# Optimization experiments

Hardware: AMD Instinct MI355X
Metric: run time of the kernel (lower is better)

Reference implementation:

```python
import math
import jax, jax.numpy as jnp
import numpy as np

B, N, D, H, NUM_N, NUM_J = 16, 1024, 128, 8, 8, 4
PRE_S = 2.0


def setup_inputs() -> dict:
    key = jax.random.key(0)
    ks = jax.random.split(key, 12)
    g = lambda i, shape: jax.random.normal(ks[i], shape, jnp.float32) * 0.02
    return {
        "eigenvector": jax.random.normal(ks[0], (B, N, N), jnp.float32),
        "eigenvalue": jax.random.uniform(ks[1], (B, N), jnp.float32, minval=0.0, maxval=2.0),
        "length": jax.random.randint(ks[2], (B,), N // 2, N).at[0].set(N),
        "eig_w_W": g(3, (D, D + 1)), "eig_w_b": jnp.zeros((D,), jnp.float32),
        "ln1_s": jnp.ones((D,), jnp.float32), "ln1_b": jnp.zeros((D,), jnp.float32),
        "ln2_s": jnp.ones((D,), jnp.float32), "ln2_b": jnp.zeros((D,), jnp.float32),
        "qkv_W": g(4, (3 * D, D)), "qkv_b": jnp.zeros((3 * D,), jnp.float32),
        "out_W": g(5, (D, D)), "out_b": jnp.zeros((D,), jnp.float32),
        "ffn_W1": g(6, (D, D)), "ffn_b1": jnp.zeros((D,), jnp.float32),
        "ffn_W2": g(7, (D, D)), "ffn_b2": jnp.zeros((D,), jnp.float32),
        "dec_sca_W": g(8, (NUM_N, D)), "dec_sca_b": jnp.zeros((NUM_N,), jnp.float32),
        "dec_wav_W": g(9, (NUM_N, D)), "dec_wav_b": jnp.zeros((NUM_N,), jnp.float32),
        "dec_scl_W": g(10, (NUM_J, D)), "dec_scl_b": jnp.zeros((NUM_J,), jnp.float32),
    }


def _layernorm(x, s, b):
    m = x.mean(-1, keepdims=True)
    v = ((x - m) ** 2).mean(-1, keepdims=True)
    return (x - m) / jnp.sqrt(v + 1e-5) * s + b


def _gen_base(y, num_n):
    # Chebyshev-style recurrence; returns (base_wavelet, base_scaling), each [B, num_n, ...y.shape[1:]]
    t_even = jnp.ones_like(y)
    t_odd = y
    wav, sca = [t_even], [t_odd]
    for _ in range(num_n - 1):
        t_even = 2.0 * y * t_odd - t_even
        t_odd = 2.0 * y * t_even - t_odd
        wav.append(t_even)
        sca.append(t_odd)
    return jnp.stack(wav, 1), jnp.stack(sca, 1)


def _forward(eigenvalue, length,
             eig_w_W, eig_w_b, ln1_s, ln1_b, ln2_s, ln2_b,
             qkv_W, qkv_b, out_W, out_b, ffn_W1, ffn_b1, ffn_W2, ffn_b2,
             dec_sca_W, dec_sca_b, dec_wav_W, dec_wav_b, dec_scl_W, dec_scl_b):
    eva = eigenvalue  # [B, N], max(length) == N by construction
    pad = jnp.arange(N)[None, :] >= length[:, None]  # [B, N], True = padded key

    # --- SineEncoding ---
    div = jnp.exp(jnp.arange(0, D, 2).astype(jnp.float32) * (-math.log(10000.0) / D))  # [D/2]
    pe = (eva * 100.0)[:, :, None] * div  # [B, N, D/2]
    eeig = jnp.concatenate([eva[:, :, None], jnp.sin(pe), jnp.cos(pe)], -1)  # [B, N, D+1]
    eig = eeig @ eig_w_W.T + eig_w_b  # [B, N, D]

    # --- MHA block (pre-norm, key padding mask) ---
    h = _layernorm(eig, ln1_s, ln1_b)
    q, k, v = jnp.split(h @ qkv_W.T + qkv_b, 3, axis=-1)
    dh = D // H
    rh = lambda t: t.reshape(B, N, H, dh)
    scores = jnp.einsum('bqhd,bkhd->bhqk', rh(q), rh(k)) / math.sqrt(dh)
    scores = jnp.where(pad[:, None, None, :], -1e9, scores)  # finite mask (padded rows zeroed later)
    attn = jax.nn.softmax(scores, axis=-1)
    mo = jnp.einsum('bhqk,bkhd->bqhd', attn, rh(v)).reshape(B, N, D) @ out_W.T + out_b
    eig = eig + mo

    # --- FFN block ---
    f = _layernorm(eig, ln2_s, ln2_b)
    f = jax.nn.gelu(f @ ffn_W1.T + ffn_b1, approximate=False) @ ffn_W2.T + ffn_b2
    eig = eig + f

    lenf = length.astype(jnp.float32)[:, None]

    def pooled(W, b):
        c = eig @ W.T + b
        c = jnp.where(pad[:, :, None], 0.0, c)
        return c.sum(1) / (lenf + 1e-8)

    coe_sca = jax.nn.sigmoid(pooled(dec_sca_W, dec_sca_b))  # [B, NUM_N]
    coe_sca = coe_sca / (coe_sca.sum(-1, keepdims=True) + 1e-8)
    coe_wav = jax.nn.sigmoid(pooled(dec_wav_W, dec_wav_b))
    coe_wav = coe_wav / (coe_wav.sum(-1, keepdims=True) + 1e-8)
    coe_scl = jax.nn.sigmoid(pooled(dec_scl_W, dec_scl_b)) * PRE_S  # [B, NUM_J]

    _, base_scaling = _gen_base(eva[:, :, None] - 1.0, NUM_N)  # [B, NUM_N, N, 1]
    fsw = eva[:, :, None] * coe_scl[:, None, :]  # [B, N, NUM_J]
    fsw = jnp.where(fsw > 2.0, 0.0, fsw)
    base_wavelet, _ = _gen_base(fsw - 1.0, NUM_N)  # [B, NUM_N, N, NUM_J]

    base_scaling = 0.5 * (1.0 - base_scaling)
    base_wavelet = 0.5 * (1.0 - base_wavelet)
    curr_s = jnp.einsum('bn,bnxj->bxj', coe_sca, base_scaling)  # [B, N, 1]
    curr_w = jnp.einsum('bn,bnxj->bxj', coe_wav, base_wavelet)  # [B, N, NUM_J]
    out = jnp.concatenate([curr_s, curr_w], -1)  # [B, N, 1+NUM_J]
    out = out / (jnp.linalg.norm(out, axis=-1, keepdims=True) + 1e-8)  # tight_frames
    return out


def reference(eigenvector, eigenvalue, length,
              eig_w_W, eig_w_b, ln1_s, ln1_b, ln2_s, ln2_b,
              qkv_W, qkv_b, out_W, out_b, ffn_W1, ffn_b1, ffn_W2, ffn_b2,
              dec_sca_W, dec_sca_b, dec_wav_W, dec_wav_b, dec_scl_W, dec_scl_b):
    # eigenvector (evc_dense) is passed through unchanged in the original; the learned
    # output is filter_signals_after, which we return.
    return _forward(eigenvalue, length,
                    eig_w_W, eig_w_b, ln1_s, ln1_b, ln2_s, ln2_b,
                    qkv_W, qkv_b, out_W, out_b, ffn_W1, ffn_b1, ffn_W2, ffn_b2,
                    dec_sca_W, dec_sca_b, dec_wav_W, dec_wav_b, dec_scl_W, dec_scl_b)
```

## Files before the change

### kernel.cpp

```cpp
#include <hip/hip_runtime.h>
#include <math.h>

#define NB 16
#define NN 1024
#define ND 128
#define NH 8
#define DH 16

typedef float f32x4 __attribute__((ext_vector_type(4)));
typedef short s16x4 __attribute__((ext_vector_type(4)));

static __device__ __forceinline__ ushort f2bf(float x) {
  unsigned u = __float_as_uint(x);
  u = (u + 0x7FFFu + ((u >> 16) & 1u)) >> 16;
  return (ushort)u;
}

static __device__ __forceinline__ float exp2h(float x) {
  return __builtin_amdgcn_exp2f(x);
}

static __device__ __forceinline__ f32x4 mfma16(s16x4 a, s16x4 b, f32x4 c) {
  return __builtin_amdgcn_mfma_f32_16x16x16bf16_1k(a, b, c, 0, 0, 0);
}

static __device__ __forceinline__ s16x4 pack_bf4(float p0, float p1, float p2,
                                                 float p3) {
  s16x4 r = {(short)f2bf(p0), (short)f2bf(p1), (short)f2bf(p2),
             (short)f2bf(p3)};
  return r;
}

#define QSCALE 0.36067376022224085f

__global__ __launch_bounds__(256) void kW(
    const float* __restrict__ eW, const float* __restrict__ qkvW,
    const float* __restrict__ outW, const float* __restrict__ W1,
    const float* __restrict__ W2, ushort* __restrict__ wbf) {
  int i = blockIdx.x * 256 + threadIdx.x;
  if (i < 18432) {
    int r = i / 144, k = i - r * 144;
    wbf[i] = (k < 129) ? f2bf(eW[r * 129 + k]) : (ushort)0;
  } else if (i < 67584) {
    wbf[i] = f2bf(qkvW[i - 18432]);
  } else if (i < 83968) {
    wbf[i] = f2bf(outW[i - 67584]);
  } else if (i < 100352) {
    wbf[i] = f2bf(W1[i - 83968]);
  } else if (i < 116736) {
    wbf[i] = f2bf(W2[i - 100352]);
  }
}

__global__ __launch_bounds__(256, 4) void kA(
    const float* __restrict__ eva, const ushort* __restrict__ eWbf,
    const float* __restrict__ eb, const float* __restrict__ g1s,
    const float* __restrict__ g1b, const ushort* __restrict__ qkvbf,
    const float* __restrict__ qb, float* __restrict__ eig,
    ushort* __restrict__ qg, ushort* __restrict__ kg,
    ushort* __restrict__ vt) {
  __shared__ __align__(16) ushort ee[32][148];
  __shared__ __align__(16) float eig_f[32][132];
  __shared__ __align__(16) ushort hbf[32][132];
  int t = threadIdx.x;
  int rows0 = blockIdx.x * 32;
  int w = t >> 6, l = t & 63, g = l >> 4, c = l & 15;

  {
    int d = t & 63, r0 = t >> 6;
    float div = __expf((float)(2 * d) * (-9.210340371976184f / 128.0f));
#pragma unroll
    for (int k = 0; k < 8; ++k) {
      int row = r0 + 4 * k;
      float e = eva[rows0 + row];
      float pe = e * 100.0f * div;
      ee[row][1 + d] = f2bf(__sinf(pe));
      ee[row][65 + d] = f2bf(__cosf(pe));
      if (d == 0) ee[row][0] = f2bf(e);
    }
  }
  for (int i = t; i < 32 * 19; i += 256) {
    int row = i / 19, cc = 129 + (i - row * 19);
    ee[row][cc] = 0;
  }
  __syncthreads();

  {
    int rt = w >> 1;
#pragma unroll
    for (int i = 0; i < 4; ++i) {
      int ct = (w & 1) * 4 + i;
      f32x4 st = {0.f, 0.f, 0.f, 0.f};
#pragma unroll
      for (int kk = 0; kk < 9; ++kk) {
        s16x4 xf = *(const s16x4*)&ee[rt * 16 + c][kk * 16 + g * 4];
        s16x4 yf = *(const s16x4*)&eWbf[(ct * 16 + c) * 144 + kk * 16 + g * 4];
        st = mfma16(xf, yf, st);
      }
      float bias = eb[ct * 16 + c];
#pragma unroll
      for (int j = 0; j < 4; ++j)
        eig_f[rt * 16 + g * 4 + j][ct * 16 + c] = st[j] + bias;
    }
  }
  __syncthreads();

#pragma unroll
  for (int p = 0; p < 4; ++p) {
    int idx = p * 256 + t;
    int row = idx >> 5, c4 = idx & 31;
    *(float4*)&eig[(size_t)(rows0 + row) * ND + c4 * 4] =
        *(const float4*)&eig_f[row][c4 * 4];
  }

  {
    int row = t >> 3, s = t & 7;
    float vals[16];
    float sum = 0.f;
#pragma unroll
    for (int k = 0; k < 16; ++k) {
      vals[k] = eig_f[row][s + 8 * k];
      sum += vals[k];
    }
    sum += __shfl_xor(sum, 1, 8);
    sum += __shfl_xor(sum, 2, 8);
    sum += __shfl_xor(sum, 4, 8);
    float mean = sum * (1.0f / 128.0f);
    float sq = 0.f;
#pragma unroll
    for (int k = 0; k < 16; ++k) {
      float d = vals[k] - mean;
      sq += d * d;
    }
    sq += __shfl_xor(sq, 1, 8);
    sq += __shfl_xor(sq, 2, 8);
    sq += __shfl_xor(sq, 4, 8);
    float rstd = rsqrtf(sq * (1.0f / 128.0f) + 1e-5f);
#pragma unroll
    for (int k = 0; k < 16; ++k) {
      int col = s + 8 * k;
      hbf[row][col] = f2bf((vals[k] - mean) * rstd * g1s[col] + g1b[col]);
    }
  }
  __syncthreads();

  {
    int rt = w >> 1;
    int b = rows0 >> 10, nn0 = rows0 & 1023;
#pragma unroll
    for (int i = 0; i < 12; ++i) {
      int ct = (w & 1) * 12 + i;
      f32x4 st = {0.f, 0.f, 0.f, 0.f};
#pragma unroll
      for (int kk = 0; kk < 8; ++kk) {
        s16x4 xf = *(const s16x4*)&hbf[rt * 16 + c][kk * 16 + g * 4];
        s16x4 yf = *(const s16x4*)&qkvbf[(ct * 16 + c) * 128 + kk * 16 + g * 4];
        st = mfma16(xf, yf, st);
      }
      float bias = qb[ct * 16 + c];
      int which = ct >> 3, head = ct & 7;
      if (which == 2) {
        unsigned lo = (unsigned)f2bf(st[0] + bias) |
                      ((unsigned)f2bf(st[1] + bias) << 16);
        unsigned hi = (unsigned)f2bf(st[2] + bias) |
                      ((unsigned)f2bf(st[3] + bias) << 16);
        uint2 pk;
        pk.x = lo;
        pk.y = hi;
        *(uint2*)(vt + ((size_t)(b * NH + head) * DH + c) * NN + nn0 +
                  rt * 16 + g * 4) = pk;
      } else {
        ushort* dst = which == 0 ? qg : kg;
        float sc = which == 0 ? QSCALE : 1.0f;
        size_t base =
            ((size_t)(b * NH + head) * NN + nn0 + rt * 16 + g * 4) * DH + c;
#pragma unroll
        for (int j = 0; j < 4; ++j)
          dst[base + j * DH] = f2bf((st[j] + bias) * sc);
      }
    }
  }
}

__global__ __launch_bounds__(512) void k_attn(
    const ushort* __restrict__ qg, const ushort* __restrict__ kg,
    const ushort* __restrict__ vt, const int* __restrict__ length,
    ushort* __restrict__ att) {
  __shared__ ushort Ksh[2][128][20];
  __shared__ ushort VTsh[2][16][136];
  int bid = blockIdx.x;
  int bh = bid >> 3, qc = bid & 7;
  int b = bh >> 3, h = bh & 7;
  int t = threadIdx.x;
  int w = t >> 6, l = t & 63, g = l >> 4, c = l & 15;
  int len = length[b];
  int nt = (len + 127) >> 7;
  int qrow = qc * 128 + w * 16 + c;
  s16x4 qf = *(const s16x4*)(qg + ((size_t)bh * NN + qrow) * DH + g * 4);
  f32x4 oacc0 = {0.f, 0.f, 0.f, 0.f};
  f32x4 oacc1 = {0.f, 0.f, 0.f, 0.f};
  float lsum = 0.f;
  int ksr = t >> 2, ksc = t & 3;
  int vr = t >> 5, vc = t & 31;
  const ushort* kbg = kg + (size_t)bh * NN * DH;
  const ushort* vbg = vt + (size_t)bh * DH * NN;

  {
    uint2 kv = *(const uint2*)(kbg + (size_t)ksr * DH + ksc * 4);
    uint2 vv = *(const uint2*)(vbg + (size_t)vr * NN + vc * 4);
    *(uint2*)&Ksh[0][ksr][ksc * 4] = kv;
    *(uint2*)&VTsh[0][vr][vc * 4] = vv;
  }
  __syncthreads();

  int cur = 0;
  for (int ti = 0; ti < nt; ++ti) {
    int t0 = ti << 7;
    bool pre = (ti + 1 < nt);
    uint2 kvn = {0u, 0u}, vvn = {0u, 0u};
    if (pre) {
      int t1 = t0 + 128;
      kvn = *(const uint2*)(kbg + (size_t)(t1 + ksr) * DH + ksc * 4);
      vvn = *(const uint2*)(vbg + (size_t)vr * NN + t1 + vc * 4);
    }
    if (t0 + 128 <= len) {
      __builtin_amdgcn_s_setprio(1);
#pragma unroll
      for (int kt = 0; kt < 8; ++kt) {
        s16x4 kf = *(const s16x4*)&Ksh[cur][kt * 16 + c][g * 4];
        f32x4 st = {0.f, 0.f, 0.f, 0.f};
        st = mfma16(kf, qf, st);
        float p0 = exp2h(st[0]), p1 = exp2h(st[1]);
        float p2 = exp2h(st[2]), p3 = exp2h(st[3]);
        lsum += (p0 + p1) + (p2 + p3);
        s16x4 pf = pack_bf4(p0, p1, p2, p3);
        s16x4 vf = *(const s16x4*)&VTsh[cur][c][kt * 16 + g * 4];
        if (kt & 1) oacc1 = mfma16(vf, pf, oacc1);
        else oacc0 = mfma16(vf, pf, oacc0);
      }
      __builtin_amdgcn_s_setprio(0);
    } else {
      for (int kt = 0; kt < 8 && t0 + kt * 16 < len; ++kt) {
        s16x4 kf = *(const s16x4*)&Ksh[cur][kt * 16 + c][g * 4];
        f32x4 st = {0.f, 0.f, 0.f, 0.f};
        st = mfma16(kf, qf, st);
        int kj = t0 + kt * 16 + g * 4;
        float p0 = (kj + 0 < len) ? exp2h(st[0]) : 0.f;
        float p1 = (kj + 1 < len) ? exp2h(st[1]) : 0.f;
        float p2 = (kj + 2 < len) ? exp2h(st[2]) : 0.f;
        float p3 = (kj + 3 < len) ? exp2h(st[3]) : 0.f;
        lsum += (p0 + p1) + (p2 + p3);
        s16x4 pf = pack_bf4(p0, p1, p2, p3);
        s16x4 vf = *(const s16x4*)&VTsh[cur][c][kt * 16 + g * 4];
        if (kt & 1) oacc1 = mfma16(vf, pf, oacc1);
        else oacc0 = mfma16(vf, pf, oacc0);
      }
    }
    if (pre) {
      *(uint2*)&Ksh[cur ^ 1][ksr][ksc * 4] = kvn;
      *(uint2*)&VTsh[cur ^ 1][vr][vc * 4] = vvn;
      __syncthreads();
      cur ^= 1;
    }
  }
  f32x4 oacc = {oacc0[0] + oacc1[0], oacc0[1] + oacc1[1],
                oacc0[2] + oacc1[2], oacc0[3] + oacc1[3]};
  lsum += __shfl_xor(lsum, 16, 64);
  lsum += __shfl_xor(lsum, 32, 64);
  float inv = 1.0f / lsum;
  s16x4 ob = pack_bf4(oacc[0] * inv, oacc[1] * inv, oacc[2] * inv,
                      oacc[3] * inv);
  *(s16x4*)(att + ((size_t)b * NN + qrow) * ND + h * DH + g * 4) = ob;
}

__global__ __launch_bounds__(256, 4) void kB(
    const ushort* __restrict__ attg, const ushort* __restrict__ outbf,
    const float* __restrict__ ob, const float* __restrict__ g2s,
    const float* __restrict__ g2b, const ushort* __restrict__ w1bf,
    const float* __restrict__ fb1, const ushort* __restrict__ w2bf,
    const float* __restrict__ fb2, const float* __restrict__ eig,
    const int* __restrict__ length, float* __restrict__ bsum) {
  __shared__ __align__(16) ushort attb[32][136];
  __shared__ __align__(16) float eig_f[32][132];
  __shared__ __align__(16) ushort hbf[32][132];
  __shared__ float csum[2][128];
  int t = threadIdx.x;
  int rows0 = blockIdx.x * 32;
  int w = t >> 6, l = t & 63, g = l >> 4, c = l & 15;
  int rt = w >> 1;

#pragma unroll
  for (int p = 0; p < 2; ++p) {
    int idx = p * 256 + t;
    int row = idx >> 4, c8 = idx & 15;
    *(uint4*)&attb[row][c8 * 8] =
        *(const uint4*)&attg[(size_t)(rows0 + row) * ND + c8 * 8];
  }
#pragma unroll
  for (int p = 0; p < 4; ++p) {
    int idx = p * 256 + t;
    int row = idx >> 5, c4 = idx & 31;
    *(float4*)&eig_f[row][c4 * 4] =
        *(const float4*)&eig[(size_t)(rows0 + row) * ND + c4 * 4];
  }
  __syncthreads();

#pragma unroll
  for (int i = 0; i < 4; ++i) {
    int ct = (w & 1) * 4 + i;
    f32x4 st = {0.f, 0.f, 0.f, 0.f};
#pragma unroll
    for (int kk = 0; kk < 8; ++kk) {
      s16x4 xf = *(const s16x4*)&attb[rt * 16 + c][kk * 16 + g * 4];
      s16x4 yf = *(const s16x4*)&outbf[(ct * 16 + c) * 128 + kk * 16 + g * 4];
      st = mfma16(xf, yf, st);
    }
    float bias = ob[ct * 16 + c];
#pragma unroll
    for (int j = 0; j < 4; ++j) {
      int row = rt * 16 + g * 4 + j, col = ct * 16 + c;
      eig_f[row][col] = st[j] + bias + eig_f[row][col];
    }
  }
  __syncthreads();

  {
    int row = t >> 3, s = t & 7;
    float vals[16];
    float sum = 0.f;
#pragma unroll
    for (int k = 0; k < 16; ++k) {
      vals[k] = eig_f[row][s + 8 * k];
      sum += vals[k];
    }
    sum += __shfl_xor(sum, 1, 8);
    sum += __shfl_xor(sum, 2, 8);
    sum += __shfl_xor(sum, 4, 8);
    float mean = sum * (1.0f / 128.0f);
    float sq = 0.f;
#pragma unroll
    for (int k = 0; k < 16; ++k) {
      float d = vals[k] - mean;
      sq += d * d;
    }
    sq += __shfl_xor(sq, 1, 8);
    sq += __shfl_xor(sq, 2, 8);
    sq += __shfl_xor(sq, 4, 8);
    float rstd = rsqrtf(sq * (1.0f / 128.0f) + 1e-5f);
#pragma unroll
    for (int k = 0; k < 16; ++k) {
      int col = s + 8 * k;
      hbf[row][col] = f2bf((vals[k] - mean) * rstd * g2s[col] + g2b[col]);
    }
  }
  __syncthreads();

#pragma unroll
  for (int i = 0; i < 4; ++i) {
    int ct = (w & 1) * 4 + i;
    f32x4 st = {0.f, 0.f, 0.f, 0.f};
#pragma unroll
    for (int kk = 0; kk < 8; ++kk) {
      s16x4 xf = *(const s16x4*)&hbf[rt * 16 + c][kk * 16 + g * 4];
      s16x4 yf = *(const s16x4*)&w1bf[(ct * 16 + c) * 128 + kk * 16 + g * 4];
      st = mfma16(xf, yf, st);
    }
    float bias = fb1[ct * 16 + c];
#pragma unroll
    for (int j = 0; j < 4; ++j) {
      float gv = st[j] + bias;
      attb[rt * 16 + g * 4 + j][ct * 16 + c] =
          f2bf(0.5f * gv * (1.0f + erff(gv * 0.7071067811865475f)));
    }
  }
  __syncthreads();

#pragma unroll
  for (int i = 0; i < 4; ++i) {
    int ct = (w & 1) * 4 + i;
    f32x4 st = {0.f, 0.f, 0.f, 0.f};
#pragma unroll
    for (int kk = 0; kk < 8; ++kk) {
      s16x4 xf = *(const s16x4*)&attb[rt * 16 + c][kk * 16 + g * 4];
      s16x4 yf = *(const s16x4*)&w2bf[(ct * 16 + c) * 128 + kk * 16 + g * 4];
      st = mfma16(xf, yf, st);
    }
    float bias = fb2[ct * 16 + c];
#pragma unroll
    for (int j = 0; j < 4; ++j) {
      int row = rt * 16 + g * 4 + j, col = ct * 16 + c;
      eig_f[row][col] = st[j] + bias + eig_f[row][col];
    }
  }
  __syncthreads();

  {
    int b = rows0 >> 10, n0 = rows0 & 1023;
    int len = length[b];
    int col = t & 127, half = t >> 7;
    float s = 0.f;
#pragma unroll
    for (int r = 0; r < 16; ++r) {
      int row = half * 16 + r;
      if (n0 + row < len) s += eig_f[row][col];
    }
    csum[half][col] = s;
  }
  __syncthreads();
  if (t < 128) bsum[(size_t)blockIdx.x * 128 + t] = csum[0][t] + csum[1][t];
}

__global__ __launch_bounds__(128) void kE(
    const float* __restrict__ bsum, const int* __restrict__ length,
    const float* __restrict__ dsW, const float* __restrict__ dsB,
    const float* __restrict__ dwW, const float* __restrict__ dwB,
    const float* __restrict__ dlW, const float* __restrict__ dlB,
    float* __restrict__ coe) {
  int b = blockIdx.x, t = threadIdx.x;
  __shared__ float s[128];
  __shared__ float pg[20];
  __shared__ float nrm[2];
  float a = 0.f;
#pragma unroll
  for (int c = 0; c < 32; ++c) a += bsum[(size_t)(b * 32 + c) * 128 + t];
  s[t] = a;
  __syncthreads();
  if (t < 20) {
    const float* W = t < 8 ? dsW + t * 128
                           : (t < 16 ? dwW + (t - 8) * 128 : dlW + (t - 16) * 128);
    float bias = t < 8 ? dsB[t] : (t < 16 ? dwB[t - 8] : dlB[t - 16]);
    float d = 0.f;
    for (int j = 0; j < 128; ++j) d += s[j] * W[j];
    float lf = (float)length[b];
    float pooled = (d + lf * bias) / (lf + 1e-8f);
    pg[t] = 1.f / (1.f + expf(-pooled));
  }
  __syncthreads();
  if (t == 0) {
    float a1 = 0.f, a2 = 0.f;
    for (int i = 0; i < 8; ++i) a1 += pg[i];
    for (int i = 8; i < 16; ++i) a2 += pg[i];
    nrm[0] = a1 + 1e-8f;
    nrm[1] = a2 + 1e-8f;
  }
  __syncthreads();
  if (t < 8) coe[b * 20 + t] = pg[t] / nrm[0];
  else if (t < 16) coe[b * 20 + t] = pg[t] / nrm[1];
  else if (t < 20) coe[b * 20 + t] = pg[t] * 2.0f;
}

__global__ __launch_bounds__(256) void k_wave(const float* __restrict__ eva,
                                              const float* __restrict__ coe,
                                              float* __restrict__ out) {
  int bn = blockIdx.x * 256 + threadIdx.x;
  int b = bn >> 10;
  float e = eva[bn];
  const float* cb = coe + b * 20;
  float y = e - 1.0f;
  float te = 1.0f, to = y;
  float cs = cb[0] * 0.5f * (1.0f - to);
#pragma unroll
  for (int i = 1; i < 8; ++i) {
    te = 2.f * y * to - te;
    to = 2.f * y * te - to;
    cs += cb[i] * 0.5f * (1.0f - to);
  }
  float cw[4];
#pragma unroll
  for (int j = 0; j < 4; ++j) {
    float fs = e * cb[16 + j];
    fs = (fs > 2.0f) ? 0.0f : fs;
    float yw = fs - 1.0f;
    float te2 = 1.0f, to2 = yw;
    float acc = 0.0f;
#pragma unroll
    for (int i = 1; i < 8; ++i) {
      te2 = 2.f * yw * to2 - te2;
      to2 = 2.f * yw * te2 - to2;
      acc += cb[8 + i] * 0.5f * (1.0f - te2);
    }
    cw[j] = acc;
  }
  float nrm = cs * cs + cw[0] * cw[0] + cw[1] * cw[1] + cw[2] * cw[2] +
              cw[3] * cw[3];
  float inv = 1.0f / (sqrtf(nrm) + 1e-8f);
  float* o = out + bn * 5;
  o[0] = cs * inv;
  o[1] = cw[0] * inv;
  o[2] = cw[1] * inv;
  o[3] = cw[2] * inv;
  o[4] = cw[3] * inv;
}

extern "C" void kernel_launch(void* const* d_in, const int* in_sizes, int n_in,
                              void* d_out, int out_size, void* d_ws,
                              size_t ws_size, hipStream_t stream) {
  const float* eva = (const float*)d_in[1];
  const int* length = (const int*)d_in[2];
  const float* eig_w_W = (const float*)d_in[3];
  const float* eig_w_b = (const float*)d_in[4];
  const float* ln1_s = (const float*)d_in[5];
  const float* ln1_b = (const float*)d_in[6];
  const float* ln2_s = (const float*)d_in[7];
  const float* ln2_b = (const float*)d_in[8];
  const float* qkv_W = (const float*)d_in[9];
  const float* qkv_b = (const float*)d_in[10];
  const float* out_W = (const float*)d_in[11];
  const float* out_b = (const float*)d_in[12];
  const float* ffn_W1 = (const float*)d_in[13];
  const float* ffn_b1 = (const float*)d_in[14];
  const float* ffn_W2 = (const float*)d_in[15];
  const float* ffn_b2 = (const float*)d_in[16];
  const float* dec_sca_W = (const float*)d_in[17];
  const float* dec_sca_b = (const float*)d_in[18];
  const float* dec_wav_W = (const float*)d_in[19];
  const float* dec_wav_b = (const float*)d_in[20];
  const float* dec_scl_W = (const float*)d_in[21];
  const float* dec_scl_b = (const float*)d_in[22];

  float* ws = (float*)d_ws;
  const size_t SZ = (size_t)NB * NN * ND;
  float* eig = ws;
  ushort* qg = (ushort*)(ws + SZ);
  ushort* kg = qg + SZ;
  ushort* vt = kg + SZ;
  ushort* attg = vt + SZ;
  float* bsum = (float*)(attg + SZ);
  float* coe = bsum + 512 * 128;
  ushort* wbf = (ushort*)(coe + 512);
  ushort* eWbf = wbf;
  ushort* qkvbf = wbf + 18432;
  ushort* outbf = wbf + 67584;
  ushort* w1bf = wbf + 83968;
  ushort* w2bf = wbf + 100352;

  kW<<<(116736 + 255) / 256, 256, 0, stream>>>(eig_w_W, qkv_W, out_W, ffn_W1,
                                               ffn_W2, wbf);
  kA<<<NB * NN / 32, 256, 0, stream>>>(eva, eWbf, eig_w_b, ln1_s, ln1_b, qkvbf,
                                       qkv_b, eig, qg, kg, vt);
  k_attn<<<NB * NH * 8, 512, 0, stream>>>(qg, kg, vt, length, attg);
  kB<<<NB * NN / 32, 256, 0, stream>>>(attg, outbf, out_b, ln2_s, ln2_b, w1bf,
                                       ffn_b1, w2bf, ffn_b2, eig, length, bsum);
  kE<<<NB, 128, 0, stream>>>(bsum, length, dec_sca_W, dec_sca_b, dec_wav_W,
                             dec_wav_b, dec_scl_W, dec_scl_b, coe);
  k_wave<<<(NB * NN) / 256, 256, 0, stream>>>(eva, coe, (float*)d_out);
}
```

Baseline: 100.2 us.

## Halve row tiles in kA/kB, use tanh GELU, fuse decoder into wave kernel

kA and kB now process 16 rows per block instead of 32, which doubles the grid and raises the occupancy hint, so more blocks are in flight. Each block reloads the bf16 weights for half as many rows, which adds weight traffic. The exact erf GELU is replaced by a tanh approximation built on exp2, which changes numerics. The kE coefficient kernel is merged into k_wave, saving one launch but making each of the four blocks per batch recompute the bsum reduction and decoder.

```diff
diff --git a/kernel.cpp b/kernel.cpp
--- a/kernel.cpp
+++ b/kernel.cpp
@@ -18,6 +18,15 @@
 
 static __device__ __forceinline__ float exp2h(float x) {
   return __builtin_amdgcn_exp2f(x);
+}
+
+static __device__ __forceinline__ float gelu_f(float x) {
+  float u = 0.7978845608028654f * (x + 0.044715f * x * x * x);
+  float au = fabsf(u);
+  float tex = exp2h(-2.8853900817779268f * au);
+  float th = (1.0f - tex) / (1.0f + tex);
+  th = copysignf(th, u);
+  return 0.5f * x * (1.0f + th);
 }
 
 static __device__ __forceinline__ f32x4 mfma16(s16x4 a, s16x4 b, f32x4 c) {
@@ -52,25 +61,25 @@
   }
 }
 
-__global__ __launch_bounds__(256, 4) void kA(
+__global__ __launch_bounds__(256, 6) void kA(
     const float* __restrict__ eva, const ushort* __restrict__ eWbf,
     const float* __restrict__ eb, const float* __restrict__ g1s,
     const float* __restrict__ g1b, const ushort* __restrict__ qkvbf,
     const float* __restrict__ qb, float* __restrict__ eig,
     ushort* __restrict__ qg, ushort* __restrict__ kg,
     ushort* __restrict__ vt) {
-  __shared__ __align__(16) ushort ee[32][148];
-  __shared__ __align__(16) float eig_f[32][132];
-  __shared__ __align__(16) ushort hbf[32][132];
+  __shared__ __align__(16) ushort ee[16][148];
+  __shared__ __align__(16) float eig_f[16][132];
+  __shared__ __align__(16) ushort hbf[16][132];
   int t = threadIdx.x;
-  int rows0 = blockIdx.x * 32;
+  int rows0 = blockIdx.x * 16;
   int w = t >> 6, l = t & 63, g = l >> 4, c = l & 15;
 
   {
     int d = t & 63, r0 = t >> 6;
     float div = __expf((float)(2 * d) * (-9.210340371976184f / 128.0f));
 #pragma unroll
-    for (int k = 0; k < 8; ++k) {
+    for (int k = 0; k < 4; ++k) {
       int row = r0 + 4 * k;
       float e = eva[rows0 + row];
       float pe = e * 100.0f * div;
@@ -79,34 +88,31 @@
       if (d == 0) ee[row][0] = f2bf(e);
     }
   }
-  for (int i = t; i < 32 * 19; i += 256) {
+  for (int i = t; i < 16 * 19; i += 256) {
     int row = i / 19, cc = 129 + (i - row * 19);
     ee[row][cc] = 0;
   }
   __syncthreads();
 
-  {
-    int rt = w >> 1;
-#pragma unroll
-    for (int i = 0; i < 4; ++i) {
-      int ct = (w & 1) * 4 + i;
-      f32x4 st = {0.f, 0.f, 0.f, 0.f};
-#pragma unroll
-      for (int kk = 0; kk < 9; ++kk) {
-        s16x4 xf = *(const s16x4*)&ee[rt * 16 + c][kk * 16 + g * 4];
-        s16x4 yf = *(const s16x4*)&eWbf[(ct * 16 + c) * 144 + kk * 16 + g * 4];
-        st = mfma16(xf, yf, st);
-      }
-      float bias = eb[ct * 16 + c];
-#pragma unroll
-      for (int j = 0; j < 4; ++j)
-        eig_f[rt * 16 + g * 4 + j][ct * 16 + c] = st[j] + bias;
-    }
-  }
-  __syncthreads();
-
-#pragma unroll
-  for (int p = 0; p < 4; ++p) {
+#pragma unroll
+  for (int i = 0; i < 2; ++i) {
+    int ct = w * 2 + i;
+    f32x4 st = {0.f, 0.f, 0.f, 0.f};
+#pragma unroll
+    for (int kk = 0; kk < 9; ++kk) {
+      s16x4 xf = *(const s16x4*)&ee[c][kk * 16 + g * 4];
+      s16x4 yf = *(const s16x4*)&eWbf[(ct * 16 + c) * 144 + kk * 16 + g * 4];
+      st = mfma16(xf, yf, st);
+    }
+    float bias = eb[ct * 16 + c];
+#pragma unroll
+    for (int j = 0; j < 4; ++j)
+      eig_f[g * 4 + j][ct * 16 + c] = st[j] + bias;
+  }
+  __syncthreads();
+
+#pragma unroll
+  for (int p = 0; p < 2; ++p) {
     int idx = p * 256 + t;
     int row = idx >> 5, c4 = idx & 31;
     *(float4*)&eig[(size_t)(rows0 + row) * ND + c4 * 4] =
@@ -114,46 +120,47 @@
   }
 
   {
-    int row = t >> 3, s = t & 7;
-    float vals[16];
+    int row = t >> 4, s = t & 15;
+    float vals[8];
     float sum = 0.f;
 #pragma unroll
-    for (int k = 0; k < 16; ++k) {
-      vals[k] = eig_f[row][s + 8 * k];
+    for (int k = 0; k < 8; ++k) {
+      vals[k] = eig_f[row][s + 16 * k];
       sum += vals[k];
     }
-    sum += __shfl_xor(sum, 1, 8);
-    sum += __shfl_xor(sum, 2, 8);
-    sum += __shfl_xor(sum, 4, 8);
+    sum += __shfl_xor(sum, 1, 16);
+    sum += __shfl_xor(sum, 2, 16);
+    sum += __shfl_xor(sum, 4, 16);
+    sum += __shfl_xor(sum, 8, 16);
     float mean = sum * (1.0f / 128.0f);
     float sq = 0.f;
 #pragma unroll
-    for (int k = 0; k < 16; ++k) {
+    for (int k = 0; k < 8; ++k) {
       float d = vals[k] - mean;
       sq += d * d;
     }
-    sq += __shfl_xor(sq, 1, 8);
-    sq += __shfl_xor(sq, 2, 8);
-    sq += __shfl_xor(sq, 4, 8);
+    sq += __shfl_xor(sq, 1, 16);
+    sq += __shfl_xor(sq, 2, 16);
+    sq += __shfl_xor(sq, 4, 16);
+    sq += __shfl_xor(sq, 8, 16);
     float rstd = rsqrtf(sq * (1.0f / 128.0f) + 1e-5f);
 #pragma unroll
-    for (int k = 0; k < 16; ++k) {
-      int col = s + 8 * k;
+    for (int k = 0; k < 8; ++k) {
+      int col = s + 16 * k;
       hbf[row][col] = f2bf((vals[k] - mean) * rstd * g1s[col] + g1b[col]);
     }
   }
   __syncthreads();
 
   {
-    int rt = w >> 1;
     int b = rows0 >> 10, nn0 = rows0 & 1023;
 #pragma unroll
-    for (int i = 0; i < 12; ++i) {
-      int ct = (w & 1) * 12 + i;
+    for (int i = 0; i < 6; ++i) {
+      int ct = w * 6 + i;
       f32x4 st = {0.f, 0.f, 0.f, 0.f};
 #pragma unroll
       for (int kk = 0; kk < 8; ++kk) {
-        s16x4 xf = *(const s16x4*)&hbf[rt * 16 + c][kk * 16 + g * 4];
+        s16x4 xf = *(const s16x4*)&hbf[c][kk * 16 + g * 4];
         s16x4 yf = *(const s16x4*)&qkvbf[(ct * 16 + c) * 128 + kk * 16 + g * 4];
         st = mfma16(xf, yf, st);
       }
@@ -167,13 +174,12 @@
         uint2 pk;
         pk.x = lo;
         pk.y = hi;
-        *(uint2*)(vt + ((size_t)(b * NH + head) * DH + c) * NN + nn0 +
-                  rt * 16 + g * 4) = pk;
+        *(uint2*)(vt + ((size_t)(b * NH + head) * DH + c) * NN + nn0 + g * 4) =
+            pk;
       } else {
         ushort* dst = which == 0 ? qg : kg;
         float sc = which == 0 ? QSCALE : 1.0f;
-        size_t base =
-            ((size_t)(b * NH + head) * NN + nn0 + rt * 16 + g * 4) * DH + c;
+        size_t base = ((size_t)(b * NH + head) * NN + nn0 + g * 4) * DH + c;
 #pragma unroll
         for (int j = 0; j < 4; ++j)
           dst[base + j * DH] = f2bf((st[j] + bias) * sc);
@@ -273,31 +279,28 @@
   *(s16x4*)(att + ((size_t)b * NN + qrow) * ND + h * DH + g * 4) = ob;
 }
 
-__global__ __launch_bounds__(256, 4) void kB(
+__global__ __launch_bounds__(256, 6) void kB(
     const ushort* __restrict__ attg, const ushort* __restrict__ outbf,
     const float* __restrict__ ob, const float* __restrict__ g2s,
     const float* __restrict__ g2b, const ushort* __restrict__ w1bf,
     const float* __restrict__ fb1, const ushort* __restrict__ w2bf,
     const float* __restrict__ fb2, const float* __restrict__ eig,
     const int* __restrict__ length, float* __restrict__ bsum) {
-  __shared__ __align__(16) ushort attb[32][136];
-  __shared__ __align__(16) float eig_f[32][132];
-  __shared__ __align__(16) ushort hbf[32][132];
+  __shared__ __align__(16) ushort attb[16][136];
+  __shared__ __align__(16) float eig_f[16][132];
+  __shared__ __align__(16) ushort hbf[16][132];
   __shared__ float csum[2][128];
   int t = threadIdx.x;
-  int rows0 = blockIdx.x * 32;
+  int rows0 = blockIdx.x * 16;
   int w = t >> 6, l = t & 63, g = l >> 4, c = l & 15;
-  int rt = w >> 1;
-
-#pragma unroll
-  for (int p = 0; p < 2; ++p) {
-    int idx = p * 256 + t;
-    int row = idx >> 4, c8 = idx & 15;
+
+  {
+    int row = t >> 4, c8 = t & 15;
     *(uint4*)&attb[row][c8 * 8] =
         *(const uint4*)&attg[(size_t)(rows0 + row) * ND + c8 * 8];
   }
 #pragma unroll
-  for (int p = 0; p < 4; ++p) {
+  for (int p = 0; p < 2; ++p) {
     int idx = p * 256 + t;
     int row = idx >> 5, c4 = idx & 31;
     *(float4*)&eig_f[row][c4 * 4] =
@@ -306,89 +309,88 @@
   __syncthreads();
 
 #pragma unroll
-  for (int i = 0; i < 4; ++i) {
-    int ct = (w & 1) * 4 + i;
+  for (int i = 0; i < 2; ++i) {
+    int ct = w * 2 + i;
     f32x4 st = {0.f, 0.f, 0.f, 0.f};
 #pragma unroll
     for (int kk = 0; kk < 8; ++kk) {
-      s16x4 xf = *(const s16x4*)&attb[rt * 16 + c][kk * 16 + g * 4];
+      s16x4 xf = *(const s16x4*)&attb[c][kk * 16 + g * 4];
       s16x4 yf = *(const s16x4*)&outbf[(ct * 16 + c) * 128 + kk * 16 + g * 4];
       st = mfma16(xf, yf, st);
     }
     float bias = ob[ct * 16 + c];
 #pragma unroll
     for (int j = 0; j < 4; ++j) {
-      int row = rt * 16 + g * 4 + j, col = ct * 16 + c;
+      int row = g * 4 + j, col = ct * 16 + c;
       eig_f[row][col] = st[j] + bias + eig_f[row][col];
     }
   }
   __syncthreads();
 
   {
-    int row = t >> 3, s = t & 7;
-    float vals[16];
+    int row = t >> 4, s = t & 15;
+    float vals[8];
     float sum = 0.f;
 #pragma unroll
-    for (int k = 0; k < 16; ++k) {
-      vals[k] = eig_f[row][s + 8 * k];
+    for (int k = 0; k < 8; ++k) {
+      vals[k] = eig_f[row][s + 16 * k];
       sum += vals[k];
     }
-    sum += __shfl_xor(sum, 1, 8);
-    sum += __shfl_xor(sum, 2, 8);
-    sum += __shfl_xor(sum, 4, 8);
+    sum += __shfl_xor(sum, 1, 16);
+    sum += __shfl_xor(sum, 2, 16);
+    sum += __shfl_xor(sum, 4, 16);
+    sum += __shfl_xor(sum, 8, 16);
     float mean = sum * (1.0f / 128.0f);
     float sq = 0.f;
 #pragma unroll
-    for (int k = 0; k < 16; ++k) {
+    for (int k = 0; k < 8; ++k) {
       float d = vals[k] - mean;
       sq += d * d;
     }
-    sq += __shfl_xor(sq, 1, 8);
-    sq += __shfl_xor(sq, 2, 8);
-    sq += __shfl_xor(sq, 4, 8);
+    sq += __shfl_xor(sq, 1, 16);
+    sq += __shfl_xor(sq, 2, 16);
+    sq += __shfl_xor(sq, 4, 16);
+    sq += __shfl_xor(sq, 8, 16);
     float rstd = rsqrtf(sq * (1.0f / 128.0f) + 1e-5f);
 #pragma unroll
-    for (int k = 0; k < 16; ++k) {
-      int col = s + 8 * k;
+    for (int k = 0; k < 8; ++k) {
+      int col = s + 16 * k;
       hbf[row][col] = f2bf((vals[k] - mean) * rstd * g2s[col] + g2b[col]);
     }
   }
   __syncthreads();
 
 #pragma unroll
-  for (int i = 0; i < 4; ++i) {
-    int ct = (w & 1) * 4 + i;
+  for (int i = 0; i < 2; ++i) {
+    int ct = w * 2 + i;
     f32x4 st = {0.f, 0.f, 0.f, 0.f};
 #pragma unroll
     for (int kk = 0; kk < 8; ++kk) {
-      s16x4 xf = *(const s16x4*)&hbf[rt * 16 + c][kk * 16 + g * 4];
+      s16x4 xf = *(const s16x4*)&hbf[c][kk * 16 + g * 4];
       s16x4 yf = *(const s16x4*)&w1bf[(ct * 16 + c) * 128 + kk * 16 + g * 4];
       st = mfma16(xf, yf, st);
     }
     float bias = fb1[ct * 16 + c];
 #pragma unroll
-    for (int j = 0; j < 4; ++j) {
-      float gv = st[j] + bias;
-      attb[rt * 16 + g * 4 + j][ct * 16 + c] =
-          f2bf(0.5f * gv * (1.0f + erff(gv * 0.7071067811865475f)));
-    }
-  }
-  __syncthreads();
-
-#pragma unroll
-  for (int i = 0; i < 4; ++i) {
-    int ct = (w & 1) * 4 + i;
+    for (int j = 0; j < 4; ++j)
+      attb[g * 4 + j][ct * 16 + c] = f2bf(gelu_f(st[j] + bias));
+  }
+  __syncthreads();
+
+#pragma unroll
+  for (int i = 0; i < 2; ++i) {
+    int ct = w * 2 + i;
     f32x4 st = {0.f, 0.f, 0.f, 0.f};
 #pragma unroll
     for (int kk = 0; kk < 8; ++kk) {
-      s16x4 xf = *(const s16x4*)&attb[rt * 16 + c][kk * 16 + g * 4];
+      s16x4 xf = *(const s16x4*)&attb[c][kk * 16 + g * 4];
       s16x4 yf = *(const s16x4*)&w2bf[(ct * 16 + c) * 128 + kk * 16 + g * 4];
       st = mfma16(xf, yf, st);
     }
     float bias = fb2[ct * 16 + c];
 #pragma unroll
     for (int j = 0; j < 4; ++j) {
-      int row = rt * 16 + g * 4 + j, col = ct * 16 + c;
+      int row = g * 4 + j, col = ct * 16 + c;
       eig_f[row][col] = st[j] + bias + eig_f[row][col];
     }
   }
@@ -400,8 +402,8 @@
     int col = t & 127, half = t >> 7;
     float s = 0.f;
 #pragma unroll
-    for (int r = 0; r < 16; ++r) {
-      int row = half * 16 + r;
+    for (int r = 0; r < 8; ++r) {
+      int row = half * 8 + r;
       if (n0 + row < len) s += eig_f[row][col];
     }
     csum[half][col] = s;
@@ -410,20 +412,24 @@
   if (t < 128) bsum[(size_t)blockIdx.x * 128 + t] = csum[0][t] + csum[1][t];
 }
 
-__global__ __launch_bounds__(128) void kE(
-    const float* __restrict__ bsum, const int* __restrict__ length,
-    const float* __restrict__ dsW, const float* __restrict__ dsB,
-    const float* __restrict__ dwW, const float* __restrict__ dwB,
-    const float* __restrict__ dlW, const float* __restrict__ dlB,
-    float* __restrict__ coe) {
-  int b = blockIdx.x, t = threadIdx.x;
+__global__ __launch_bounds__(256) void k_wave(
+    const float* __restrict__ eva, const float* __restrict__ bsum,
+    const int* __restrict__ length, const float* __restrict__ dsW,
+    const float* __restrict__ dsB, const float* __restrict__ dwW,
+    const float* __restrict__ dwB, const float* __restrict__ dlW,
+    const float* __restrict__ dlB, float* __restrict__ out) {
   __shared__ float s[128];
   __shared__ float pg[20];
   __shared__ float nrm[2];
-  float a = 0.f;
-#pragma unroll
-  for (int c = 0; c < 32; ++c) a += bsum[(size_t)(b * 32 + c) * 128 + t];
-  s[t] = a;
+  __shared__ float cb[20];
+  int t = threadIdx.x;
+  int b = blockIdx.x >> 2;
+  if (t < 128) {
+    float a = 0.f;
+#pragma unroll
+    for (int c = 0; c < 64; ++c) a += bsum[(size_t)(b * 64 + c) * 128 + t];
+    s[t] = a;
+  }
   __syncthreads();
   if (t < 20) {
     const float* W = t < 8 ? dsW + t * 128
@@ -444,18 +450,13 @@
     nrm[1] = a2 + 1e-8f;
   }
   __syncthreads();
-  if (t < 8) coe[b * 20 + t] = pg[t] / nrm[0];
-  else if (t < 16) coe[b * 20 + t] = pg[t] / nrm[1];
-  else if (t < 20) coe[b * 20 + t] = pg[t] * 2.0f;
-}
-
-__global__ __launch_bounds__(256) void k_wave(const float* __restrict__ eva,
-                                              const float* __restrict__ coe,
-                                              float* __restrict__ out) {
-  int bn = blockIdx.x * 256 + threadIdx.x;
-  int b = bn >> 10;
+  if (t < 8) cb[t] = pg[t] / nrm[0];
+  else if (t < 16) cb[t] = pg[t] / nrm[1];
+  else if (t < 20) cb[t] = pg[t] * 2.0f;
+  __syncthreads();
+
+  int bn = blockIdx.x * 256 + t;
   float e = eva[bn];
-  const float* cb = coe + b * 20;
   float y = e - 1.0f;
   float te = 1.0f, to = y;
   float cs = cb[0] * 0.5f * (1.0f - to);
@@ -481,9 +482,9 @@
     }
     cw[j] = acc;
   }
-  float nrm = cs * cs + cw[0] * cw[0] + cw[1] * cw[1] + cw[2] * cw[2] +
-              cw[3] * cw[3];
-  float inv = 1.0f / (sqrtf(nrm) + 1e-8f);
+  float nr = cs * cs + cw[0] * cw[0] + cw[1] * cw[1] + cw[2] * cw[2] +
+             cw[3] * cw[3];
+  float inv = 1.0f / (sqrtf(nr) + 1e-8f);
   float* o = out + bn * 5;
   o[0] = cs * inv;
   o[1] = cw[0] * inv;
@@ -526,8 +527,7 @@
   ushort* vt = kg + SZ;
   ushort* attg = vt + SZ;
   float* bsum = (float*)(attg + SZ);
-  float* coe = bsum + 512 * 128;
-  ushort* wbf = (ushort*)(coe + 512);
+  ushort* wbf = (ushort*)(bsum + 1024 * 128);
   ushort* eWbf = wbf;
   ushort* qkvbf = wbf + 18432;
   ushort* outbf = wbf + 67584;
@@ -536,12 +536,13 @@
 
   kW<<<(116736 + 255) / 256, 256, 0, stream>>>(eig_w_W, qkv_W, out_W, ffn_W1,
                                                ffn_W2, wbf);
-  kA<<<NB * NN / 32, 256, 0, stream>>>(eva, eWbf, eig_w_b, ln1_s, ln1_b, qkvbf,
+  kA<<<NB * NN / 16, 256, 0, stream>>>(eva, eWbf, eig_w_b, ln1_s, ln1_b, qkvbf,
                                        qkv_b, eig, qg, kg, vt);
   k_attn<<<NB * NH * 8, 512, 0, stream>>>(qg, kg, vt, length, attg);
-  kB<<<NB * NN / 32, 256, 0, stream>>>(attg, outbf, out_b, ln2_s, ln2_b, w1bf,
+  kB<<<NB * NN / 16, 256, 0, stream>>>(attg, outbf, out_b, ln2_s, ln2_b, w1bf,
                                        ffn_b1, w2bf, ffn_b2, eig, length, bsum);
-  kE<<<NB, 128, 0, stream>>>(bsum, length, dec_sca_W, dec_sca_b, dec_wav_W,
-                             dec_wav_b, dec_scl_W, dec_scl_b, coe);
-  k_wave<<<(NB * NN) / 256, 256, 0, stream>>>(eva, coe, (float*)d_out);
-}
+  k_wave<<<(NB * NN) / 256, 256, 0, stream>>>(eva, bsum, length, dec_sca_W,
+                                              dec_sca_b, dec_wav_W, dec_wav_b,
+                                              dec_scl_W, dec_scl_b,
+                                              (float*)d_out);
+}
```

After: 109.6 us. +9.4%, slower.
